# Optimization experiments

Measured on AMD Instinct MI355X. Metric: run time of the kernel, lower is better.

The kernel has to match this reference:

```python
import jax, jax.numpy as jnp
import numpy as np

N, E, D, H, ED = 50000, 150000, 128, 4, 16


def _ln(x, g, b, eps=1e-5):
    m = jnp.mean(x, -1, keepdims=True)
    v = jnp.var(x, -1, keepdims=True)
    return (x - m) / jnp.sqrt(v + eps) * g + b


def _seg_softmax(logits, seg, n):
    # numerically stable softmax over edges grouped by destination node
    m = jax.ops.segment_max(logits, seg, num_segments=n)
    e = jnp.exp(logits - m[seg])
    s = jax.ops.segment_sum(e, seg, num_segments=n)
    return e / (s[seg] + 1e-16)


def setup_inputs():
    key = jax.random.key(0)
    ks = jax.random.split(key, 16)
    def w(i, shape, s=0.05):
        return jax.random.normal(ks[i], shape, jnp.float32) * s
    return dict(
        x=w(0, (N, D), 1.0),
        edge_index=jax.random.randint(ks[1], (2, E), 0, N),
        edge_attr=w(2, (E, ED), 1.0),
        sage_Wl=w(3, (D, D)), sage_Wr=w(4, (D, D)), sage_b=jnp.zeros((D,), jnp.float32),
        tq_W=w(5, (D, H * D)), tq_b=jnp.zeros((H * D,), jnp.float32),
        tk_W=w(6, (D, H * D)), tk_b=jnp.zeros((H * D,), jnp.float32),
        tv_W=w(7, (D, H * D)), tv_b=jnp.zeros((H * D,), jnp.float32),
        te_W=w(8, (ED, H * D)),
        tskip_W=w(9, (D, D)), tskip_b=jnp.zeros((D,), jnp.float32),
        gat_W=w(10, (D, H * D)), gat_att_src=w(11, (H, D)), gat_att_dst=w(12, (H, D)),
        gat_bias=jnp.zeros((D,), jnp.float32),
        gate_short=jnp.ones((1,), jnp.float32), gate_attn=jnp.ones((1,), jnp.float32),
        gate_neighbor=jnp.ones((1,), jnp.float32),
        fus_W=w(13, (3 * D, D)), fus_b=jnp.zeros((D,), jnp.float32),
        fus_g=jnp.ones((D,), jnp.float32), fus_beta=jnp.zeros((D,), jnp.float32),
        norm_g=jnp.ones((D,), jnp.float32), norm_b=jnp.zeros((D,), jnp.float32),
    )


def reference(x, edge_index, edge_attr, sage_Wl, sage_Wr, sage_b,
              tq_W, tq_b, tk_W, tk_b, tv_W, tv_b, te_W, tskip_W, tskip_b,
              gat_W, gat_att_src, gat_att_dst, gat_bias,
              gate_short, gate_attn, gate_neighbor,
              fus_W, fus_b, fus_g, fus_beta, norm_g, norm_b):
    n, d = x.shape
    h = tq_W.shape[1] // d
    src, dst = edge_index[0], edge_index[1]

    # --- SAGEConv: mean aggregation of neighbors + root linear ---
    agg = jax.ops.segment_sum(x[src], dst, num_segments=n)
    cnt = jax.ops.segment_sum(jnp.ones((src.shape[0],), x.dtype), dst, num_segments=n)
    mean = agg / jnp.maximum(cnt, 1.0)[:, None]
    x_short = jax.nn.relu(mean @ sage_Wl + x @ sage_Wr + sage_b)

    # --- TransformerConv (concat=False, edge-conditioned key/value, skip) ---
    q = (x @ tq_W + tq_b).reshape(n, h, d)
    k = (x @ tk_W + tk_b).reshape(n, h, d)
    v = (x @ tv_W + tv_b).reshape(n, h, d)
    e = (edge_attr @ te_W).reshape(-1, h, d)           # [E,H,d]
    logits = jnp.sum(q[dst] * (k[src] + e), -1) / np.float32(np.sqrt(d))  # [E,H]
    alpha = _seg_softmax(logits, dst, n)
    out_t = jax.ops.segment_sum((v[src] + e) * alpha[..., None], dst, num_segments=n).mean(1)
    x_attn = jax.nn.relu(out_t + x @ tskip_W + tskip_b)

    # --- GATConv (adds self-loops, concat=False averages heads, bias) ---
    loops = jnp.arange(n)
    s2 = jnp.concatenate([src, loops])
    d2 = jnp.concatenate([dst, loops])
    g = (x @ gat_W).reshape(n, h, d)
    a_s = jnp.sum(g * gat_att_src, -1)                 # [N,H]
    a_d = jnp.sum(g * gat_att_dst, -1)
    lg = jax.nn.leaky_relu(a_s[s2] + a_d[d2], 0.2)     # [E+N,H]
    al = _seg_softmax(lg, d2, n)
    out_g = jax.ops.segment_sum(g[s2] * al[..., None], d2, num_segments=n).mean(1) + gat_bias
    x_nb = jax.nn.relu(out_g)

    # --- gated fusion + residual LayerNorm ---
    gs = jax.nn.sigmoid(gate_short)
    ga = jax.nn.sigmoid(gate_attn)
    gn = jax.nn.sigmoid(gate_neighbor)
    cat = jnp.concatenate([x_short * gs, x_attn * ga, x_nb * gn], -1)
    fused = jax.nn.relu(_ln(cat @ fus_W + fus_b, fus_g, fus_beta))
    return _ln(x + fused, norm_g, norm_b)
```

## Files before the change

kernel.cpp:

```cpp
#include <hip/hip_runtime.h>
#include <hip/hip_bf16.h>

using bf16 = __hip_bfloat16;
typedef __attribute__((ext_vector_type(8))) short short8;
typedef __attribute__((ext_vector_type(4))) float f32x4;
typedef __attribute__((ext_vector_type(4))) unsigned short u16x4;

__device__ __forceinline__ void store4(bf16* p, float v0, float v1, float v2, float v3) {
    u16x4 pk;
    bf16 h0 = __float2bfloat16(v0); pk[0] = *(unsigned short*)&h0;
    bf16 h1 = __float2bfloat16(v1); pk[1] = *(unsigned short*)&h1;
    bf16 h2 = __float2bfloat16(v2); pk[2] = *(unsigned short*)&h2;
    bf16 h3 = __float2bfloat16(v3); pk[3] = *(unsigned short*)&h3;
    *(u16x4*)p = pk;
}
__device__ __forceinline__ float b2f(short s) { bf16 h; *(short*)&h = s; return __bfloat162float(h); }

__device__ __forceinline__ size_t pidx(int c, int k, int K) {
    return ((size_t)(((c >> 6) * (K >> 5) + (k >> 5)) * 4 + ((c >> 4) & 3)) * 64
            + (((k >> 3) & 3) * 16 + (c & 15))) * 8 + (k & 7);
}

__global__ __launch_bounds__(256) void zero_ws(unsigned* p, size_t n) {
    size_t i = (size_t)blockIdx.x * 256 + threadIdx.x;
    size_t stride = (size_t)gridDim.x * 256;
    for (; i < n; i += stride) p[i] = 0u;
}

__global__ __launch_bounds__(256) void prep_all(
    const float* __restrict__ x, bf16* __restrict__ x_b,
    bf16* __restrict__ Wt_sage, const float* __restrict__ sage_Wl, const float* __restrict__ sage_Wr,
    bf16* __restrict__ Wt_fus, const float* __restrict__ fus_W,
    const float* __restrict__ gate_s, const float* __restrict__ gate_a, const float* __restrict__ gate_n,
    bf16* __restrict__ Wt_cat, const float* __restrict__ tvW,
    const float* __restrict__ tskipW, const float* __restrict__ teW,
    bf16* __restrict__ Wgag, const float* __restrict__ gatW,
    float* __restrict__ bvsum, const float* __restrict__ tvb, int ND)
{
    const int TP = 128 * 128;
    long i = (long)blockIdx.x * 256 + threadIdx.x;
    long nv = ND >> 3;
    if (i < nv) {
        long b = i * 8;
        f32x4 a0 = *(const f32x4*)(x + b);
        f32x4 a1 = *(const f32x4*)(x + b + 4);
        short8 o;
        #pragma unroll
        for (int j = 0; j < 4; ++j) { bf16 h = __float2bfloat16(a0[j]); o[j] = *(short*)&h; }
        #pragma unroll
        for (int j = 0; j < 4; ++j) { bf16 h = __float2bfloat16(a1[j]); o[4 + j] = *(short*)&h; }
        *(short8*)(x_b + b) = o;
        return;
    }
    i -= nv;
    if (i < TP) { int k = (int)i / 128, c = (int)i % 128; Wt_sage[pidx(c, k, 256)] = __float2bfloat16(sage_Wl[i]); return; }
    i -= TP;
    if (i < TP) { int k = (int)i / 128, c = (int)i % 128; Wt_sage[pidx(c, k + 128, 256)] = __float2bfloat16(sage_Wr[i]); return; }
    i -= TP;
    if (i < 3 * TP) {
        int sseg = (int)(i / TP); int r = (int)(i % TP);
        int k = r / 128, c = r % 128;
        const float* g = sseg == 0 ? gate_s : (sseg == 1 ? gate_a : gate_n);
        float gv = 1.0f / (1.0f + expf(-g[0]));
        Wt_fus[pidx(c, sseg * 128 + k, 384)] = __float2bfloat16(fus_W[(size_t)sseg * TP + r] * gv);
        return;
    }
    i -= 3L * TP;
    if (i < 128L * 704) {
        int d = (int)(i / 704), kk = (int)(i % 704);
        float v;
        if (kk < 512)      { int h = kk >> 7, k = kk & 127; v = 0.25f * tvW[k * 512 + h * 128 + d]; }
        else if (kk < 640) { int k = kk - 512;              v = tskipW[k * 128 + d]; }
        else               { int t = kk - 640; int h = t >> 4, j = t & 15; v = 0.25f * teW[j * 512 + h * 128 + d]; }
        Wt_cat[pidx(d, kk, 704)] = __float2bfloat16(v);
        return;
    }
    i -= 128L * 704;
    if (i < 128L * 512) {
        int d = (int)i >> 9, k = (int)i & 511;
        int h = k >> 7, i2 = k & 127;
        Wgag[pidx(d, k, 512)] = __float2bfloat16(0.25f * gatW[(size_t)i2 * 512 + h * 128 + d]);
        return;
    }
    i -= 128L * 512;
    if (i < 128) {
        int d = (int)i;
        bvsum[d] = 0.25f * (tvb[d] + tvb[128 + d] + tvb[256 + d] + tvb[384 + d]);
    }
}

__global__ __launch_bounds__(128) void build_wbig(
    bf16* __restrict__ Wbig, float* __restrict__ bbig,
    const float* __restrict__ Wq, const float* __restrict__ Wk,
    const float* __restrict__ teW, const float* __restrict__ bq,
    const float* __restrict__ bk, const float* __restrict__ gatW,
    const float* __restrict__ attS, const float* __restrict__ attD)
{
    int c = blockIdx.x;
    int ip = threadIdx.x;
    float acc = 0.f, bacc = 0.f;
    if (c < 512) {
        int h = c >> 7, i2 = c & 127;
        const float* wkrow = Wk + (size_t)i2 * 512 + h * 128;
        const float* wqrow = Wq + (size_t)ip * 512 + h * 128;
        for (int o = 0; o < 128; ++o) acc += wqrow[o] * wkrow[o];
        if (ip == 0) { const float* bqr = bq + h * 128; for (int o = 0; o < 128; ++o) bacc += bqr[o] * wkrow[o]; }
    } else if (c < 576) {
        int t = c - 512; int h = t >> 4, j = t & 15;
        const float* terow = teW + (size_t)j * 512 + h * 128;
        const float* wqrow = Wq + (size_t)ip * 512 + h * 128;
        for (int o = 0; o < 128; ++o) acc += wqrow[o] * terow[o];
        if (ip == 0) { const float* bqr = bq + h * 128; for (int o = 0; o < 128; ++o) bacc += bqr[o] * terow[o]; }
    } else if (c < 580) {
        int h = c - 576;
        const float* bkr = bk + h * 128;
        const float* wqrow = Wq + (size_t)ip * 512 + h * 128;
        for (int o = 0; o < 128; ++o) acc += wqrow[o] * bkr[o];
        if (ip == 0) { const float* bqr = bq + h * 128; for (int o = 0; o < 128; ++o) bacc += bqr[o] * bkr[o]; }
    } else if (c < 584) {
        int h = c - 580;
        const float* ar = attS + h * 128;
        const float* gr = gatW + (size_t)ip * 512 + h * 128;
        for (int d = 0; d < 128; ++d) acc += gr[d] * ar[d];
    } else if (c < 588) {
        int h = c - 584;
        const float* ar = attD + h * 128;
        const float* gr = gatW + (size_t)ip * 512 + h * 128;
        for (int d = 0; d < 128; ++d) acc += gr[d] * ar[d];
    }
    Wbig[pidx(c, ip, 128)] = __float2bfloat16(acc);
    if (ip == 0) bbig[c] = bacc;
}

__global__ __launch_bounds__(256) void k_hist(const int* __restrict__ dst, int* __restrict__ deg_i, int E) {
    int e = blockIdx.x * 256 + threadIdx.x;
    if (e < E) atomicAdd(&deg_i[dst[e]], 1);
}

__global__ __launch_bounds__(256) void k_scan1(
    const int* __restrict__ deg_i, int* __restrict__ loc, int* __restrict__ partial, int N)
{
    __shared__ int sm[256];
    int t = threadIdx.x, i = blockIdx.x * 256 + t;
    int v = (i < N) ? deg_i[i] : 0;
    sm[t] = v;
    __syncthreads();
    for (int off = 1; off < 256; off <<= 1) {
        int add = (t >= off) ? sm[t - off] : 0;
        __syncthreads();
        sm[t] += add;
        __syncthreads();
    }
    if (i < N) loc[i] = sm[t] - v;
    if (t == 255) partial[blockIdx.x] = sm[255];
}

__global__ __launch_bounds__(256) void k_scan2(int* __restrict__ partial, int nb) {
    __shared__ int sm[256];
    int t = threadIdx.x;
    int v = (t < nb) ? partial[t] : 0;
    sm[t] = v;
    __syncthreads();
    for (int off = 1; off < 256; off <<= 1) {
        int add = (t >= off) ? sm[t - off] : 0;
        __syncthreads();
        sm[t] += add;
        __syncthreads();
    }
    if (t < nb) partial[t] = sm[t] - v;
}

__global__ __launch_bounds__(256) void k_scan3(
    const int* __restrict__ loc, const int* __restrict__ partial,
    int* __restrict__ rowptr, int* __restrict__ cursor, int N)
{
    int i = blockIdx.x * 256 + threadIdx.x;
    if (i >= N) return;
    int r = loc[i] + partial[blockIdx.x];
    rowptr[i] = r;
    cursor[i] = r;
}

__global__ __launch_bounds__(256) void k_scatter(
    const int* __restrict__ src, const int* __restrict__ dst,
    int* __restrict__ cursor, int* __restrict__ col_src, int* __restrict__ eidx, int E)
{
    int e = blockIdx.x * 256 + threadIdx.x;
    if (e >= E) return;
    int d = dst[e];
    int pos = atomicAdd(&cursor[d], 1);
    col_src[pos] = src[e];
    eidx[pos] = e;
}

__global__ __launch_bounds__(128) void gemm_wide(
    const bf16* __restrict__ A, const bf16* __restrict__ Wt,
    const float* __restrict__ bias, bf16* __restrict__ C, int n_rows, int ldc)
{
    int row0 = blockIdx.x * 64;
    int wave = threadIdx.x >> 6, lane = threadIdx.x & 63;
    int lrow = lane & 15, quad = lane >> 4;
    short8 xb[4][4];
    #pragma unroll
    for (int ks = 0; ks < 4; ++ks)
        #pragma unroll
        for (int nt = 0; nt < 4; ++nt) {
            int r = row0 + nt * 16 + lrow;
            r = r < n_rows ? r : n_rows - 1;
            xb[ks][nt] = *(const short8*)(A + (size_t)r * 128 + ks * 32 + quad * 8);
        }
    int c64 = blockIdx.y * 2 + wave;
    int cbase = c64 * 64;
    f32x4 acc[4][4] = {};
    #pragma unroll
    for (int ks = 0; ks < 4; ++ks) {
        short8 wf[4];
        #pragma unroll
        for (int mt = 0; mt < 4; ++mt)
            wf[mt] = *(const short8*)(Wt + ((size_t)((c64 * 4 + ks) * 4 + mt) * 64 + lane) * 8);
        #pragma unroll
        for (int mt = 0; mt < 4; ++mt)
            #pragma unroll
            for (int nt = 0; nt < 4; ++nt)
                acc[mt][nt] = __builtin_amdgcn_mfma_f32_16x16x32_bf16(wf[mt], xb[ks][nt], acc[mt][nt], 0, 0, 0);
    }
    #pragma unroll
    for (int nt = 0; nt < 4; ++nt) {
        int row = row0 + nt * 16 + lrow;
        if (row >= n_rows) continue;
        #pragma unroll
        for (int mt = 0; mt < 4; ++mt) {
            int col = cbase + mt * 16 + quad * 4;
            float b0 = 0.f, b1 = 0.f, b2 = 0.f, b3 = 0.f;
            if (bias) { b0 = bias[col]; b1 = bias[col + 1]; b2 = bias[col + 2]; b3 = bias[col + 3]; }
            store4(&C[(size_t)row * ldc + col],
                   acc[mt][nt][0] + b0, acc[mt][nt][1] + b1,
                   acc[mt][nt][2] + b2, acc[mt][nt][3] + b3);
        }
    }
}

#define NCAP 8
__global__ __launch_bounds__(256) void node_fused(
    const bf16* __restrict__ QT, const bf16* __restrict__ x_b,
    const float* __restrict__ edge_attr,
    const int* __restrict__ rowptr, const int* __restrict__ deg_i,
    const int* __restrict__ col_src, const int* __restrict__ eidx,
    bf16* __restrict__ mean_b, bf16* __restrict__ xa, bf16* __restrict__ ga,
    bf16* __restrict__ ea_b, int N)
{
    __shared__ short8 xS[4][NCAP][16];
    __shared__ float eaS[4][NCAP][16];
    __shared__ float wTs[4][NCAP][4];
    __shared__ float wGs[4][NCAP][4];
    int w = threadIdx.x >> 6, l = threadIdx.x & 63;
    int n = blockIdx.x * 4 + w;
    if (n >= N) return;
    int j = l & 15, g4 = l >> 4;
    int p0 = rowptr[n], dg = deg_i[n];
    const float scale = 0.08838834764831845f;
    float qtF[4][8], qeqL[4], qbL[4], adh[4], ashn[4];
    #pragma unroll
    for (int h = 0; h < 4; ++h) {
        short8 q = *(const short8*)(QT + (size_t)n * 640 + h * 128 + j * 8);
        #pragma unroll
        for (int t = 0; t < 8; ++t) qtF[h][t] = b2f(q[t]);
        qeqL[h] = __bfloat162float(QT[(size_t)n * 640 + 512 + h * 16 + j]);
        qbL[h]  = __bfloat162float(QT[(size_t)n * 640 + 576 + h]);
        ashn[h] = __bfloat162float(QT[(size_t)n * 640 + 580 + h]);
        adh[h]  = __bfloat162float(QT[(size_t)n * 640 + 584 + h]);
    }
    float xn0 = __bfloat162float(x_b[(size_t)n * 128 + l]);
    float xn1 = __bfloat162float(x_b[(size_t)n * 128 + l + 64]);
    float s_t[4], s_g[4], xaacc[8] = {}, gaacc[8];
    float mean0 = 0.f, mean1 = 0.f, eaacc = 0.f;
    #pragma unroll
    for (int h = 0; h < 4; ++h) {
        s_t[h] = 0.f;
        float lgs = ashn[h] + adh[h];
        lgs = lgs > 0.f ? lgs : 0.2f * lgs;
        float e = __expf(lgs);
        s_g[h] = e;
        gaacc[h * 2] = e * xn0; gaacc[h * 2 + 1] = e * xn1;
    }
    for (int c0 = 0; c0 < dg; c0 += NCAP) {
        int cc = min(NCAP, dg - c0);
        for (int it = 0; it < ((cc + 3) >> 2); ++it) {
            int i = it * 4 + g4;
            bool valid = i < cc;
            int s = 0;
            short8 xf = {0, 0, 0, 0, 0, 0, 0, 0};
            float ea_j = 0.f;
            if (valid) {
                s = col_src[p0 + c0 + i];
                int eg = eidx[p0 + c0 + i];
                xf = *(const short8*)(x_b + (size_t)s * 128 + j * 8);
                ea_j = edge_attr[(size_t)eg * 16 + j];
                xS[w][i][j] = xf;
                eaS[w][i][j] = ea_j;
            }
            float xv[8];
            #pragma unroll
            for (int t = 0; t < 8; ++t) xv[t] = b2f(xf[t]);
            float p[4];
            #pragma unroll
            for (int h = 0; h < 4; ++h) {
                float a = ea_j * qeqL[h];
                #pragma unroll
                for (int t = 0; t < 8; ++t) a += xv[t] * qtF[h][t];
                p[h] = a;
            }
            #pragma unroll
            for (int off = 1; off < 16; off <<= 1)
                #pragma unroll
                for (int h = 0; h < 4; ++h)
                    p[h] += __shfl_xor(p[h], off, 64);
            if (valid && j == 0) {
                #pragma unroll
                for (int h = 0; h < 4; ++h) {
                    wTs[w][i][h] = __expf((p[h] + qbL[h]) * scale);
                    float as_s = __bfloat162float(QT[(size_t)s * 640 + 580 + h]);
                    float lg = as_s + adh[h];
                    lg = lg > 0.f ? lg : 0.2f * lg;
                    wGs[w][i][h] = __expf(lg);
                }
            }
        }
        for (int i = 0; i < cc; ++i) {
            const bf16* xr = (const bf16*)&xS[w][i][0];
            float xv0 = __bfloat162float(xr[l]);
            float xv1 = __bfloat162float(xr[l + 64]);
            mean0 += xv0; mean1 += xv1;
            #pragma unroll
            for (int h = 0; h < 4; ++h) {
                float at = wTs[w][i][h], ag = wGs[w][i][h];
                s_t[h] += at; s_g[h] += ag;
                xaacc[h * 2] += at * xv0; xaacc[h * 2 + 1] += at * xv1;
                gaacc[h * 2] += ag * xv0; gaacc[h * 2 + 1] += ag * xv1;
            }
            eaacc += wTs[w][i][g4] * eaS[w][i][j];
        }
    }
    float invd = 1.f / fmaxf((float)dg, 1.f);
    mean_b[(size_t)n * 128 + l]      = __float2bfloat16(mean0 * invd);
    mean_b[(size_t)n * 128 + l + 64] = __float2bfloat16(mean1 * invd);
    #pragma unroll
    for (int h = 0; h < 4; ++h) {
        float it = 1.f / (s_t[h] + 1e-16f);
        xa[(size_t)n * 512 + h * 128 + l]      = __float2bfloat16(xaacc[h * 2] * it);
        xa[(size_t)n * 512 + h * 128 + l + 64] = __float2bfloat16(xaacc[h * 2 + 1] * it);
        float ig = 1.f / (s_g[h] + 1e-16f);
        ga[(size_t)n * 512 + h * 128 + l]      = __float2bfloat16(gaacc[h * 2] * ig);
        ga[(size_t)n * 512 + h * 128 + l + 64] = __float2bfloat16(gaacc[h * 2 + 1] * ig);
    }
    ea_b[(size_t)n * 64 + l] = __float2bfloat16(eaacc / (s_t[g4] + 1e-16f));
}

#define MFMA_ACC(ACC) \
    _Pragma("unroll") \
    for (int mt = 0; mt < 4; ++mt) \
        _Pragma("unroll") \
        for (int nt = 0; nt < 4; ++nt) \
            ACC[mt][nt] = __builtin_amdgcn_mfma_f32_16x16x32_bf16(wf[mt], xf[nt], ACC[mt][nt], 0, 0, 0);

#define FUSE_SEG(SEG) do { \
    _Pragma("unroll") \
    for (int ks = 0; ks < 4; ++ks) { \
        int kT = ks * 32 + quad * 8; \
        short8 xf[4], wf[4]; \
        _Pragma("unroll") \
        for (int t = 0; t < 4; ++t) { \
            int row_l = t * 16 + lrow; \
            xf[t] = *(const short8*)(tileb + row_l * 256 + ((kT * 2) ^ ((row_l & 7) << 4))); \
        } \
        _Pragma("unroll") \
        for (int mt = 0; mt < 4; ++mt) \
            wf[mt] = *(const short8*)(Wt_fus + ((size_t)((wave * 12 + (SEG) * 4 + ks) * 4 + mt) * 64 + lane) * 8); \
        MFMA_ACC(facc) \
    } \
} while (0)

#define STASH(BIASP, USE_BV) do { \
    _Pragma("unroll") \
    for (int nt = 0; nt < 4; ++nt) { \
        int row_l = nt * 16 + lrow; \
        int sw = (row_l & 7) << 4; \
        float bvf = (USE_BV) ? ((deg_i[rA[nt]] > 0) ? 1.f : 0.f) : 0.f; \
        _Pragma("unroll") \
        for (int mt = 0; mt < 4; ++mt) { \
            int col = cbase + mt * 16 + quad * 4; \
            f32x4 bb = *(const f32x4*)((BIASP) + col); \
            u16x4 pk; \
            _Pragma("unroll") \
            for (int jj = 0; jj < 4; ++jj) { \
                float v = acc[mt][nt][jj] + bb[jj]; \
                if (USE_BV) v += bvf * bvsum[col + jj]; \
                bf16 h = __float2bfloat16(fmaxf(v, 0.f)); \
                pk[jj] = *(unsigned short*)&h; \
            } \
            *(u16x4*)(tileb + row_l * 256 + ((col * 2) ^ sw)) = pk; \
        } \
    } \
} while (0)

__global__ __launch_bounds__(128) void tail_fused(
    const bf16* __restrict__ mean_b, const bf16* __restrict__ x_b,
    const bf16* __restrict__ ga, const bf16* __restrict__ xa,
    const bf16* __restrict__ ea_b, const int* __restrict__ deg_i,
    const float* __restrict__ x,
    const bf16* __restrict__ Wt_sage, const bf16* __restrict__ Wgag,
    const bf16* __restrict__ Wt_cat, const bf16* __restrict__ Wt_fus,
    const float* __restrict__ sage_b, const float* __restrict__ gat_bias,
    const float* __restrict__ tskip_b, const float* __restrict__ bvsum,
    const float* __restrict__ fus_b, const float* __restrict__ fus_g,
    const float* __restrict__ fus_beta, const float* __restrict__ norm_g,
    const float* __restrict__ norm_b,
    float* __restrict__ out, int N)
{
    __shared__ __align__(16) char tileb[64 * 256];
    __shared__ float2 st1[2][64];
    __shared__ float2 st2[2][64];
    int wave = threadIdx.x >> 6, lane = threadIdx.x & 63;
    int lrow = lane & 15, quad = lane >> 4;
    int row0 = blockIdx.x * 64;
    int cbase = wave * 64;
    int rA[4];
    #pragma unroll
    for (int t = 0; t < 4; ++t) {
        int r = row0 + t * 16 + lrow;
        rA[t] = r < N ? r : N - 1;
    }
    f32x4 facc[4][4] = {};

    {
        f32x4 acc[4][4] = {};
        for (int ks = 0; ks < 8; ++ks) {
            const bf16* A = (ks < 4) ? mean_b : x_b;
            int kA = (ks & 3) * 32 + quad * 8;
            short8 xf[4], wf[4];
            #pragma unroll
            for (int t = 0; t < 4; ++t)
                xf[t] = *(const short8*)(A + (size_t)rA[t] * 128 + kA);
            #pragma unroll
            for (int mt = 0; mt < 4; ++mt)
                wf[mt] = *(const short8*)(Wt_sage + ((size_t)((wave * 8 + ks) * 4 + mt) * 64 + lane) * 8);
            MFMA_ACC(acc)
        }
        STASH(sage_b, 0);
    }
    __syncthreads();
    FUSE_SEG(0);
    __syncthreads();

    {
        f32x4 acc[4][4] = {};
        for (int ks = 0; ks < 22; ++ks) {
            int kq = quad * 8;
            short8 xf[4], wf[4];
            #pragma unroll
            for (int t = 0; t < 4; ++t) {
                if (ks < 16) {
                    xf[t] = *(const short8*)(xa + (size_t)rA[t] * 512 + ks * 32 + kq);
                } else if (ks < 20) {
                    xf[t] = *(const short8*)(x_b + (size_t)rA[t] * 128 + (ks - 16) * 32 + kq);
                } else {
                    xf[t] = *(const short8*)(ea_b + (size_t)rA[t] * 64 + (ks - 20) * 32 + kq);
                }
            }
            #pragma unroll
            for (int mt = 0; mt < 4; ++mt)
                wf[mt] = *(const short8*)(Wt_cat + ((size_t)((wave * 22 + ks) * 4 + mt) * 64 + lane) * 8);
            MFMA_ACC(acc)
        }
        STASH(tskip_b, 1);
    }
    __syncthreads();
    FUSE_SEG(1);
    __syncthreads();

    {
        f32x4 acc[4][4] = {};
        for (int ks = 0; ks < 16; ++ks) {
            int k = ks * 32 + quad * 8;
            short8 xf[4], wf[4];
            #pragma unroll
            for (int t = 0; t < 4; ++t)
                xf[t] = *(const short8*)(ga + (size_t)rA[t] * 512 + k);
            #pragma unroll
            for (int mt = 0; mt < 4; ++mt)
                wf[mt] = *(const short8*)(Wgag + ((size_t)((wave * 16 + ks) * 4 + mt) * 64 + lane) * 8);
            MFMA_ACC(acc)
        }
        STASH(gat_bias, 0);
    }
    __syncthreads();
    FUSE_SEG(2);

    #pragma unroll
    for (int nt = 0; nt < 4; ++nt) {
        float s = 0.f, q = 0.f;
        #pragma unroll
        for (int mt = 0; mt < 4; ++mt) {
            int col = cbase + mt * 16 + quad * 4;
            f32x4 bb = *(const f32x4*)(fus_b + col);
            #pragma unroll
            for (int jj = 0; jj < 4; ++jj) {
                float v = facc[mt][nt][jj] + bb[jj];
                facc[mt][nt][jj] = v;
                s += v; q += v * v;
            }
        }
        s += __shfl_xor(s, 16, 64); q += __shfl_xor(q, 16, 64);
        s += __shfl_xor(s, 32, 64); q += __shfl_xor(q, 32, 64);
        if (quad == 0) st1[wave][nt * 16 + lrow] = make_float2(s, q);
    }
    __syncthreads();
    float m1[4], inv1[4];
    #pragma unroll
    for (int nt = 0; nt < 4; ++nt) {
        float2 a = st1[0][nt * 16 + lrow], b = st1[1][nt * 16 + lrow];
        float S = a.x + b.x, Q = a.y + b.y;
        float m = S * (1.f / 128.f);
        m1[nt] = m;
        inv1[nt] = rsqrtf(Q * (1.f / 128.f) - m * m + 1e-5f);
    }
    #pragma unroll
    for (int nt = 0; nt < 4; ++nt) {
        float s = 0.f, q = 0.f;
        #pragma unroll
        for (int mt = 0; mt < 4; ++mt) {
            int col = cbase + mt * 16 + quad * 4;
            f32x4 gv = *(const f32x4*)(fus_g + col);
            f32x4 bv = *(const f32x4*)(fus_beta + col);
            f32x4 xv = *(const f32x4*)(x + (size_t)rA[nt] * 128 + col);
            #pragma unroll
            for (int jj = 0; jj < 4; ++jj) {
                float y = fmaxf((facc[mt][nt][jj] - m1[nt]) * inv1[nt] * gv[jj] + bv[jj], 0.f);
                float z = xv[jj] + y;
                facc[mt][nt][jj] = z;
                s += z; q += z * z;
            }
        }
        s += __shfl_xor(s, 16, 64); q += __shfl_xor(q, 16, 64);
        s += __shfl_xor(s, 32, 64); q += __shfl_xor(q, 32, 64);
        if (quad == 0) st2[wave][nt * 16 + lrow] = make_float2(s, q);
    }
    __syncthreads();
    #pragma unroll
    for (int nt = 0; nt < 4; ++nt) {
        int row = row0 + nt * 16 + lrow;
        if (row >= N) continue;
        float2 a = st2[0][nt * 16 + lrow], b = st2[1][nt * 16 + lrow];
        float S = a.x + b.x, Q = a.y + b.y;
        float m = S * (1.f / 128.f);
        float inv = rsqrtf(Q * (1.f / 128.f) - m * m + 1e-5f);
        #pragma unroll
        for (int mt = 0; mt < 4; ++mt) {
            int col = cbase + mt * 16 + quad * 4;
            f32x4 ngv = *(const f32x4*)(norm_g + col);
            f32x4 nbv = *(const f32x4*)(norm_b + col);
            f32x4 o;
            #pragma unroll
            for (int jj = 0; jj < 4; ++jj)
                o[jj] = (facc[mt][nt][jj] - m) * inv * ngv[jj] + nbv[jj];
            *(f32x4*)(out + (size_t)row * 128 + col) = o;
        }
    }
}

extern "C" void kernel_launch(void* const* d_in, const int* in_sizes, int n_in,
                              void* d_out, int out_size, void* d_ws, size_t ws_size,
                              hipStream_t stream)
{
    const float* x        = (const float*)d_in[0];
    const int*   ei       = (const int*)d_in[1];
    const float* edge_attr= (const float*)d_in[2];
    const float* sage_Wl  = (const float*)d_in[3];
    const float* sage_Wr  = (const float*)d_in[4];
    const float* sage_b   = (const float*)d_in[5];
    const float* tq_W     = (const float*)d_in[6];
    const float* tq_b     = (const float*)d_in[7];
    const float* tk_W     = (const float*)d_in[8];
    const float* tk_b     = (const float*)d_in[9];
    const float* tv_W     = (const float*)d_in[10];
    const float* tv_b     = (const float*)d_in[11];
    const float* te_W     = (const float*)d_in[12];
    const float* tskip_W  = (const float*)d_in[13];
    const float* tskip_b  = (const float*)d_in[14];
    const float* gat_W    = (const float*)d_in[15];
    const float* att_s_w  = (const float*)d_in[16];
    const float* att_d_w  = (const float*)d_in[17];
    const float* gat_bias = (const float*)d_in[18];
    const float* gate_s   = (const float*)d_in[19];
    const float* gate_a   = (const float*)d_in[20];
    const float* gate_n   = (const float*)d_in[21];
    const float* fus_W    = (const float*)d_in[22];
    const float* fus_b    = (const float*)d_in[23];
    const float* fus_g    = (const float*)d_in[24];
    const float* fus_beta = (const float*)d_in[25];
    const float* norm_g   = (const float*)d_in[26];
    const float* norm_b   = (const float*)d_in[27];

    int N = in_sizes[0] / 128;
    int E = in_sizes[2] / 16;
    const int* src = ei;
    const int* dst = ei + E;
    int ND = N * 128;
    int nb = (N + 255) / 256;

    char* wsb = (char*)d_ws;
    size_t off = 0;
    auto carve = [&](size_t bytes) -> char* {
        char* p = wsb + off;
        off += (bytes + 255) & ~(size_t)255;
        return p;
    };
    int*   deg_i   = (int*)carve((size_t)N * 4);
    size_t zero_bytes = off;
    int*   rowptr  = (int*)carve((size_t)N * 4);
    int*   cursor  = (int*)carve((size_t)N * 4);
    int*   loc     = (int*)carve((size_t)N * 4);
    int*   partial = (int*)carve((size_t)256 * 4);
    int*   col_src = (int*)carve((size_t)E * 4);
    int*   eidx    = (int*)carve((size_t)E * 4);
    bf16*  x_b     = (bf16*)carve((size_t)N * 128 * 2);
    bf16*  QT      = (bf16*)carve((size_t)N * 640 * 2);
    bf16*  xa      = (bf16*)carve((size_t)N * 512 * 2);
    bf16*  ga      = (bf16*)carve((size_t)N * 512 * 2);
    bf16*  mean_b  = (bf16*)carve((size_t)N * 128 * 2);
    bf16*  ea_b    = (bf16*)carve((size_t)N * 64 * 2);
    bf16*  Wbig    = (bf16*)carve((size_t)640 * 128 * 2);
    float* bbig    = (float*)carve((size_t)640 * 4);
    bf16*  Wt_sage = (bf16*)carve((size_t)128 * 256 * 2);
    bf16*  Wt_fus  = (bf16*)carve((size_t)128 * 384 * 2);
    bf16*  Wt_cat  = (bf16*)carve((size_t)128 * 704 * 2);
    bf16*  Wgag    = (bf16*)carve((size_t)128 * 512 * 2);
    float* bvsum   = (float*)carve((size_t)128 * 4);

    zero_ws<<<256, 256, 0, stream>>>((unsigned*)wsb, zero_bytes / 4);
    const long TP = 128 * 128;
    long prep_total = (long)(ND >> 3) + 5L * TP + 128L * 704 + 128L * 512 + 128;
    int prep_blocks = (int)((prep_total + 255) / 256);
    prep_all<<<prep_blocks, 256, 0, stream>>>(
        x, x_b, Wt_sage, sage_Wl, sage_Wr, Wt_fus, fus_W, gate_s, gate_a, gate_n,
        Wt_cat, tv_W, tskip_W, te_W, Wgag, gat_W, bvsum, tv_b, ND);
    build_wbig<<<640, 128, 0, stream>>>(Wbig, bbig, tq_W, tk_W, te_W, tq_b, tk_b,
                                        gat_W, att_s_w, att_d_w);

    k_hist<<<(E + 255) / 256, 256, 0, stream>>>(dst, deg_i, E);
    k_scan1<<<nb, 256, 0, stream>>>(deg_i, loc, partial, N);
    k_scan2<<<1, 256, 0, stream>>>(partial, nb);
    k_scan3<<<nb, 256, 0, stream>>>(loc, partial, rowptr, cursor, N);
    k_scatter<<<(E + 255) / 256, 256, 0, stream>>>(src, dst, cursor, col_src, eidx, E);

    int gy64 = (N + 63) / 64, gnode = (N + 3) / 4;

    gemm_wide<<<dim3(gy64, 5), 128, 0, stream>>>(x_b, Wbig, bbig, QT, N, 640);

    node_fused<<<gnode, 256, 0, stream>>>(QT, x_b, edge_attr, rowptr, deg_i, col_src, eidx,
                                          mean_b, xa, ga, ea_b, N);

    tail_fused<<<gy64, 128, 0, stream>>>(
        mean_b, x_b, ga, xa, ea_b, deg_i, x,
        Wt_sage, Wgag, Wt_cat, Wt_fus,
        sage_b, gat_bias, tskip_b, bvsum,
        fus_b, fus_g, fus_beta, norm_g, norm_b,
        (float*)d_out, N);
}
```

Before: 374.6 us.

## Double-buffer GEMM operand loads through LDS via async global_load_lds

Replaces direct register loads of weights and activations in gemm_wide and tail_fused with a two-stage pipeline. Each step issues asynchronous global-to-LDS copies for the next step while the current one feeds the MFMAs. gemm_wide also drops its 5-way grid split over column blocks, so each block loops over all 640 columns and loads its A rows only once. The cost is a full vmcnt(0) wait every step, extra LDS traffic, and five times fewer blocks in gemm_wide, which may reduce occupancy and latency hiding.

After: 371.5 us. About the same (-0.8%).

```diff
diff --git a/kernel.cpp b/kernel.cpp
--- a/kernel.cpp
+++ b/kernel.cpp
@@ -15,6 +15,13 @@
     *(u16x4*)p = pk;
 }
 __device__ __forceinline__ float b2f(short s) { bf16 h; *(short*)&h = s; return __bfloat162float(h); }
+
+__device__ __forceinline__ void ld_lds16(void* lds, const void* g) {
+    __builtin_amdgcn_global_load_lds(
+        (const __attribute__((address_space(1))) unsigned int*)g,
+        (__attribute__((address_space(3))) unsigned int*)lds,
+        16, 0, 0);
+}
 
 __device__ __forceinline__ size_t pidx(int c, int k, int K) {
     return ((size_t)(((c >> 6) * (K >> 5) + (k >> 5)) * 4 + ((c >> 4) & 3)) * 64
@@ -197,6 +204,7 @@
     const bf16* __restrict__ A, const bf16* __restrict__ Wt,
     const float* __restrict__ bias, bf16* __restrict__ C, int n_rows, int ldc)
 {
+    __shared__ __align__(16) short8 wstg[2][2][4][64];
     int row0 = blockIdx.x * 64;
     int wave = threadIdx.x >> 6, lane = threadIdx.x & 63;
     int lrow = lane & 15, quad = lane >> 4;
@@ -209,33 +217,46 @@
             r = r < n_rows ? r : n_rows - 1;
             xb[ks][nt] = *(const short8*)(A + (size_t)r * 128 + ks * 32 + quad * 8);
         }
-    int c64 = blockIdx.y * 2 + wave;
-    int cbase = c64 * 64;
-    f32x4 acc[4][4] = {};
-    #pragma unroll
-    for (int ks = 0; ks < 4; ++ks) {
-        short8 wf[4];
+    auto issueW = [&](int c64, int ks, int par) {
         #pragma unroll
         for (int mt = 0; mt < 4; ++mt)
-            wf[mt] = *(const short8*)(Wt + ((size_t)((c64 * 4 + ks) * 4 + mt) * 64 + lane) * 8);
-        #pragma unroll
-        for (int mt = 0; mt < 4; ++mt)
-            #pragma unroll
-            for (int nt = 0; nt < 4; ++nt)
-                acc[mt][nt] = __builtin_amdgcn_mfma_f32_16x16x32_bf16(wf[mt], xb[ks][nt], acc[mt][nt], 0, 0, 0);
-    }
-    #pragma unroll
-    for (int nt = 0; nt < 4; ++nt) {
-        int row = row0 + nt * 16 + lrow;
-        if (row >= n_rows) continue;
-        #pragma unroll
-        for (int mt = 0; mt < 4; ++mt) {
-            int col = cbase + mt * 16 + quad * 4;
-            float b0 = 0.f, b1 = 0.f, b2 = 0.f, b3 = 0.f;
-            if (bias) { b0 = bias[col]; b1 = bias[col + 1]; b2 = bias[col + 2]; b3 = bias[col + 3]; }
-            store4(&C[(size_t)row * ldc + col],
-                   acc[mt][nt][0] + b0, acc[mt][nt][1] + b1,
-                   acc[mt][nt][2] + b2, acc[mt][nt][3] + b3);
+            ld_lds16(&wstg[wave][par][mt][0], Wt + ((size_t)((c64 * 4 + ks) * 4 + mt) * 64 + lane) * 8);
+    };
+    issueW(wave, 0, 0);
+    int stp = 0;
+    for (int cy = 0; cy < 5; ++cy) {
+        int c64 = cy * 2 + wave;
+        f32x4 acc[4][4] = {};
+        #pragma unroll
+        for (int ks = 0; ks < 4; ++ks) {
+            int par = stp & 1;
+            asm volatile("s_waitcnt vmcnt(0)" ::: "memory");
+            int nst = stp + 1;
+            if (nst < 20) issueW((nst >> 2) * 2 + wave, nst & 3, par ^ 1);
+            short8 wf[4];
+            #pragma unroll
+            for (int mt = 0; mt < 4; ++mt) wf[mt] = wstg[wave][par][mt][lane];
+            #pragma unroll
+            for (int mt = 0; mt < 4; ++mt)
+                #pragma unroll
+                for (int nt = 0; nt < 4; ++nt)
+                    acc[mt][nt] = __builtin_amdgcn_mfma_f32_16x16x32_bf16(wf[mt], xb[ks][nt], acc[mt][nt], 0, 0, 0);
+            ++stp;
+        }
+        int cbase = c64 * 64;
+        #pragma unroll
+        for (int nt = 0; nt < 4; ++nt) {
+            int row = row0 + nt * 16 + lrow;
+            if (row >= n_rows) continue;
+            #pragma unroll
+            for (int mt = 0; mt < 4; ++mt) {
+                int col = cbase + mt * 16 + quad * 4;
+                float b0 = 0.f, b1 = 0.f, b2 = 0.f, b3 = 0.f;
+                if (bias) { b0 = bias[col]; b1 = bias[col + 1]; b2 = bias[col + 2]; b3 = bias[col + 3]; }
+                store4(&C[(size_t)row * ldc + col],
+                       acc[mt][nt][0] + b0, acc[mt][nt][1] + b1,
+                       acc[mt][nt][2] + b2, acc[mt][nt][3] + b3);
+            }
         }
     }
 }
@@ -355,30 +376,6 @@
     }
     ea_b[(size_t)n * 64 + l] = __float2bfloat16(eaacc / (s_t[g4] + 1e-16f));
 }
-
-#define MFMA_ACC(ACC) \
-    _Pragma("unroll") \
-    for (int mt = 0; mt < 4; ++mt) \
-        _Pragma("unroll") \
-        for (int nt = 0; nt < 4; ++nt) \
-            ACC[mt][nt] = __builtin_amdgcn_mfma_f32_16x16x32_bf16(wf[mt], xf[nt], ACC[mt][nt], 0, 0, 0);
-
-#define FUSE_SEG(SEG) do { \
-    _Pragma("unroll") \
-    for (int ks = 0; ks < 4; ++ks) { \
-        int kT = ks * 32 + quad * 8; \
-        short8 xf[4], wf[4]; \
-        _Pragma("unroll") \
-        for (int t = 0; t < 4; ++t) { \
-            int row_l = t * 16 + lrow; \
-            xf[t] = *(const short8*)(tileb + row_l * 256 + ((kT * 2) ^ ((row_l & 7) << 4))); \
-        } \
-        _Pragma("unroll") \
-        for (int mt = 0; mt < 4; ++mt) \
-            wf[mt] = *(const short8*)(Wt_fus + ((size_t)((wave * 12 + (SEG) * 4 + ks) * 4 + mt) * 64 + lane) * 8); \
-        MFMA_ACC(facc) \
-    } \
-} while (0)
 
 #define STASH(BIASP, USE_BV) do { \
     _Pragma("unroll") \
@@ -418,10 +415,12 @@
     float* __restrict__ out, int N)
 {
     __shared__ __align__(16) char tileb[64 * 256];
+    __shared__ __align__(16) short8 stg[2][2][8][64];
     __shared__ float2 st1[2][64];
     __shared__ float2 st2[2][64];
     int wave = threadIdx.x >> 6, lane = threadIdx.x & 63;
     int lrow = lane & 15, quad = lane >> 4;
+    int kq = quad * 8;
     int row0 = blockIdx.x * 64;
     int cbase = wave * 64;
     int rA[4];
@@ -432,69 +431,109 @@
     }
     f32x4 facc[4][4] = {};
 
+    auto issueA = [&](const bf16* base, int ldA, int kA, int par) {
+        #pragma unroll
+        for (int t = 0; t < 4; ++t)
+            ld_lds16(&stg[wave][par][t][0], base + (size_t)rA[t] * ldA + kA);
+    };
+    auto issueW = [&](const bf16* Wt, int stepIdx, int par) {
+        #pragma unroll
+        for (int mt = 0; mt < 4; ++mt)
+            ld_lds16(&stg[wave][par][4 + mt][0], Wt + ((size_t)(stepIdx * 4 + mt) * 64 + lane) * 8);
+    };
+    auto mfstep = [&](f32x4 (&acc)[4][4], int par) {
+        short8 xf[4], wf[4];
+        #pragma unroll
+        for (int t = 0; t < 4; ++t) { xf[t] = stg[wave][par][t][lane]; wf[t] = stg[wave][par][4 + t][lane]; }
+        #pragma unroll
+        for (int mt = 0; mt < 4; ++mt)
+            #pragma unroll
+            for (int nt = 0; nt < 4; ++nt)
+                acc[mt][nt] = __builtin_amdgcn_mfma_f32_16x16x32_bf16(wf[mt], xf[nt], acc[mt][nt], 0, 0, 0);
+    };
+    auto fuse_seg = [&](int SEG) {
+        issueW(Wt_fus, wave * 12 + SEG * 4, 0);
+        for (int ks = 0; ks < 4; ++ks) {
+            int cur = ks & 1;
+            asm volatile("s_waitcnt vmcnt(0)" ::: "memory");
+            if (ks + 1 < 4) issueW(Wt_fus, wave * 12 + SEG * 4 + ks + 1, cur ^ 1);
+            int kT = ks * 32 + kq;
+            short8 xf[4], wf[4];
+            #pragma unroll
+            for (int t = 0; t < 4; ++t) {
+                int row_l = t * 16 + lrow;
+                xf[t] = *(const short8*)(tileb + row_l * 256 + ((kT * 2) ^ ((row_l & 7) << 4)));
+            }
+            #pragma unroll
+            for (int mt = 0; mt < 4; ++mt) wf[mt] = stg[wave][cur][4 + mt][lane];
+            #pragma unroll
+            for (int mt = 0; mt < 4; ++mt)
+                #pragma unroll
+                for (int nt = 0; nt < 4; ++nt)
+                    facc[mt][nt] = __builtin_amdgcn_mfma_f32_16x16x32_bf16(wf[mt], xf[nt], facc[mt][nt], 0, 0, 0);
+        }
+    };
+
     {
         f32x4 acc[4][4] = {};
+        issueA(mean_b, 128, kq, 0);
+        issueW(Wt_sage, wave * 8, 0);
         for (int ks = 0; ks < 8; ++ks) {
-            const bf16* A = (ks < 4) ? mean_b : x_b;
-            int kA = (ks & 3) * 32 + quad * 8;
-            short8 xf[4], wf[4];
-            #pragma unroll
-            for (int t = 0; t < 4; ++t)
-                xf[t] = *(const short8*)(A + (size_t)rA[t] * 128 + kA);
-            #pragma unroll
-            for (int mt = 0; mt < 4; ++mt)
-                wf[mt] = *(const short8*)(Wt_sage + ((size_t)((wave * 8 + ks) * 4 + mt) * 64 + lane) * 8);
-            MFMA_ACC(acc)
+            int cur = ks & 1;
+            asm volatile("s_waitcnt vmcnt(0)" ::: "memory");
+            if (ks + 1 < 8) {
+                int p = ks + 1;
+                issueA((p < 4) ? mean_b : x_b, 128, (p & 3) * 32 + kq, cur ^ 1);
+                issueW(Wt_sage, wave * 8 + p, cur ^ 1);
+            }
+            mfstep(acc, cur);
         }
         STASH(sage_b, 0);
     }
     __syncthreads();
-    FUSE_SEG(0);
+    fuse_seg(0);
     __syncthreads();
 
     {
         f32x4 acc[4][4] = {};
+        issueA(xa, 512, kq, 0);
+        issueW(Wt_cat, wave * 22, 0);
         for (int ks = 0; ks < 22; ++ks) {
-            int kq = quad * 8;
-            short8 xf[4], wf[4];
-            #pragma unroll
-            for (int t = 0; t < 4; ++t) {
-                if (ks < 16) {
-                    xf[t] = *(const short8*)(xa + (size_t)rA[t] * 512 + ks * 32 + kq);
-                } else if (ks < 20) {
-                    xf[t] = *(const short8*)(x_b + (size_t)rA[t] * 128 + (ks - 16) * 32 + kq);
-                } else {
-                    xf[t] = *(const short8*)(ea_b + (size_t)rA[t] * 64 + (ks - 20) * 32 + kq);
-                }
-            }
-            #pragma unroll
-            for (int mt = 0; mt < 4; ++mt)
-                wf[mt] = *(const short8*)(Wt_cat + ((size_t)((wave * 22 + ks) * 4 + mt) * 64 + lane) * 8);
-            MFMA_ACC(acc)
+            int cur = ks & 1;
+            asm volatile("s_waitcnt vmcnt(0)" ::: "memory");
+            if (ks + 1 < 22) {
+                int p = ks + 1;
+                if (p < 16)      issueA(xa,   512, p * 32 + kq,        cur ^ 1);
+                else if (p < 20) issueA(x_b,  128, (p - 16) * 32 + kq, cur ^ 1);
+                else             issueA(ea_b,  64, (p - 20) * 32 + kq, cur ^ 1);
+                issueW(Wt_cat, wave * 22 + p, cur ^ 1);
+            }
+            mfstep(acc, cur);
         }
         STASH(tskip_b, 1);
     }
     __syncthreads();
-    FUSE_SEG(1);
+    fuse_seg(1);
     __syncthreads();
 
     {
         f32x4 acc[4][4] = {};
+        issueA(ga, 512, kq, 0);
+        issueW(Wgag, wave * 16, 0);
         for (int ks = 0; ks < 16; ++ks) {
-            int k = ks * 32 + quad * 8;
-            short8 xf[4], wf[4];
-            #pragma unroll
-            for (int t = 0; t < 4; ++t)
-                xf[t] = *(const short8*)(ga + (size_t)rA[t] * 512 + k);
-            #pragma unroll
-            for (int mt = 0; mt < 4; ++mt)
-                wf[mt] = *(const short8*)(Wgag + ((size_t)((wave * 16 + ks) * 4 + mt) * 64 + lane) * 8);
-            MFMA_ACC(acc)
+            int cur = ks & 1;
+            asm volatile("s_waitcnt vmcnt(0)" ::: "memory");
+            if (ks + 1 < 16) {
+                int p = ks + 1;
+                issueA(ga, 512, p * 32 + kq, cur ^ 1);
+                issueW(Wgag, wave * 16 + p, cur ^ 1);
+            }
+            mfstep(acc, cur);
         }
         STASH(gat_bias, 0);
     }
     __syncthreads();
-    FUSE_SEG(2);
+    fuse_seg(2);
 
     #pragma unroll
     for (int nt = 0; nt < 4; ++nt) {
@@ -655,7 +694,7 @@
 
     int gy64 = (N + 63) / 64, gnode = (N + 3) / 4;
 
-    gemm_wide<<<dim3(gy64, 5), 128, 0, stream>>>(x_b, Wbig, bbig, QT, N, 640);
+    gemm_wide<<<gy64, 128, 0, stream>>>(x_b, Wbig, bbig, QT, N, 640);
 
     node_fused<<<gnode, 256, 0, stream>>>(QT, x_b, edge_attr, rowptr, deg_i, col_src, eidx,
                                           mean_b, xa, ga, ea_b, N);
```
